# Kernel optimization log

Hardware: AMD Instinct MI355X
Metric: run time of the kernel (lower is better)

## Reference

```python
import jax, jax.numpy as jnp
import numpy as np

CONF_THRES = 0.25   # NMS.conf
IOU_THRES = 0.45    # NMS.iou
MAX_NMS = 1024      # fixed candidate count so greedy NMS is jit-compatible
IMG = 640.0


def setup_inputs() -> dict:
    key = jax.random.key(0)
    k0, k1, k2, k3, k4 = jax.random.split(key, 5)
    B, N = 32, 25200
    cxcy = jax.random.uniform(k0, (B, N, 2), dtype=jnp.float32) * IMG
    wh = jax.random.uniform(k1, (B, N, 2), dtype=jnp.float32) * 80.0 + 2.0
    obj = jax.random.uniform(k2, (B, N, 1), dtype=jnp.float32)
    lmk = jax.random.uniform(k3, (B, N, 10), dtype=jnp.float32) * IMG
    cls = jax.random.uniform(k4, (B, N, 1), dtype=jnp.float32)
    # layout: [cx, cy, w, h, obj, 10 landmark coords, 1 class score]
    prediction = jnp.concatenate([cxcy, wh, obj, lmk, cls], axis=2)
    return {"prediction": prediction}


def xywh2xyxy(x):
    cx, cy, w, h = x[:, 0], x[:, 1], x[:, 2], x[:, 3]
    return jnp.stack([cx - w / 2, cy - h / 2, cx + w / 2, cy + h / 2], axis=1)


def pairwise_iou(b):  # b: [K,4] xyxy -> [K,K]
    area = (b[:, 2] - b[:, 0]) * (b[:, 3] - b[:, 1])
    lt = jnp.maximum(b[:, None, :2], b[None, :, :2])
    rb = jnp.minimum(b[:, None, 2:], b[None, :, 2:])
    wh = jnp.clip(rb - lt, 0.0)
    inter = wh[..., 0] * wh[..., 1]
    return inter / (area[:, None] + area[None, :] - inter + 1e-7)


def _nms_image(pred):  # pred: [N,16]
    obj = pred[:, 4]
    score = pred[:, 15] * obj  # x[:,15:] *= x[:,4:5]; nc==1 -> single class, j==0
    valid = (obj > CONF_THRES) & (score > CONF_THRES)  # xc filter + conf filter
    s = jnp.where(valid, score, -1.0)
    top_s, idx = jax.lax.top_k(s, MAX_NMS)  # score-sorted candidates (greedy NMS order)
    x = pred[idx]  # [K,16]
    box = xywh2xyxy(x[:, :4])
    vmask = top_s > 0.0  # valid candidates (invalid slots carry score -1)
    # class offset c = j*4096 is identically 0 since nc==1 -> skip
    iou = pairwise_iou(box)  # [K,K]
    rng = jnp.arange(MAX_NMS)

    def step(keep, i):
        sup = keep[i] & (iou[i] > IOU_THRES) & (rng > i)
        return keep & ~sup, None

    keep, _ = jax.lax.scan(step, vmask, rng)
    det = jnp.concatenate(
        [box, top_s[:, None], x[:, 5:15], jnp.zeros((MAX_NMS, 1), pred.dtype)], axis=1
    )  # [K,16] = box(4) | conf(1) | landmarks(10) | class(1)=0
    return det * keep[:, None].astype(det.dtype), keep


def reference(prediction):
    # Fixed-shape analogue of the per-image ragged output: detections padded to
    # MAX_NMS rows per image (zeroed where suppressed) plus a keep mask.
    det, keep = jax.vmap(_nms_image)(prediction)
    return det, keep
```

## Files before the change

kernel.cpp:

```cpp
#include <hip/hip_runtime.h>
#include <stdint.h>

#define NB 32
#define NN 25200
#define NN4 6300
#define TOPK 1024
#define NF 16
#define CONF 0.25f
#define IOU_T 0.45f
#define NBIN 4096
#define CAP 2048
#define KEY_BASE 0xBE800001u
#define PITCH 257

__device__ __forceinline__ uint32_t score_key(float obj, float cls) {
  float score = __fmul_rn(cls, obj);
  bool valid = (obj > CONF) && (score > CONF);
  float s = valid ? score : -1.0f;
  uint32_t u = __float_as_uint(s);
  return (u & 0x80000000u) ? ~u : (u | 0x80000000u);
}

__device__ __forceinline__ uint64_t shfl_xor_u64(uint64_t v, int m) {
  uint32_t lo = __shfl_xor((uint32_t)v, m, 64);
  uint32_t hi = __shfl_xor((uint32_t)(v >> 32), m, 64);
  return ((uint64_t)hi << 32) | lo;
}

__global__ void k_keys(const float* __restrict__ pred, uint32_t* __restrict__ keys,
                       uint32_t* __restrict__ cnt) {
  if (blockIdx.x == 0 && threadIdx.x < NB) cnt[threadIdx.x] = 0u;
  int g = blockIdx.x * blockDim.x + threadIdx.x;
  if (g >= NB * NN) return;
  const float* row = pred + (size_t)g * NF;
  keys[g] = score_key(row[4], row[15]);
}

__global__ __launch_bounds__(1024) void k_select(const float* __restrict__ pred,
                                                 const uint32_t* __restrict__ keys,
                                                 int* __restrict__ sel,
                                                 float4* __restrict__ boxv,
                                                 float* __restrict__ arv,
                                                 uint32_t* __restrict__ vb) {
  int b = blockIdx.x;
  int tid = threadIdx.x;
  int lane = tid & 63, wid = tid >> 6;
  const uint4* kb4 = (const uint4*)(keys + (size_t)b * NN);
  __shared__ uint32_t hist[NBIN];
  __shared__ uint64_t ent[CAP];
  __shared__ uint32_t wsum[16];
  __shared__ uint32_t sh_bin;
  __shared__ uint32_t sh_cnt;
  #pragma unroll
  for (int k = 0; k < 4; ++k) hist[tid + 1024 * k] = 0;
  ent[tid] = 0; ent[tid + 1024] = 0;
  if (tid == 0) { sh_cnt = 0; sh_bin = 0; }
  __syncthreads();

  uint4 kreg[7];
  #pragma unroll
  for (int k = 0; k < 7; ++k) {
    int i = tid + k * 1024;
    if (i < NN4) {
      kreg[k] = kb4[i];
      uint32_t kv[4] = {kreg[k].x, kreg[k].y, kreg[k].z, kreg[k].w};
      #pragma unroll
      for (int c = 0; c < 4; ++c) {
        uint32_t key = kv[c];
        if (key >= KEY_BASE) {
          uint32_t bin = (key - KEY_BASE) >> 12;
          if (bin > NBIN - 1) bin = NBIN - 1;
          atomicAdd(&hist[bin], 1u);
        }
      }
    }
  }
  __syncthreads();

  uint32_t h[4]; uint32_t s = 0;
  #pragma unroll
  for (int k = 0; k < 4; ++k) { h[k] = hist[NBIN - 1 - (4 * tid + k)]; s += h[k]; }
  uint32_t my = s;
  #pragma unroll
  for (int d = 1; d < 64; d <<= 1) {
    uint32_t v = __shfl_up(s, d, 64);
    if (lane >= d) s += v;
  }
  if (lane == 63) wsum[wid] = s;
  __syncthreads();
  uint32_t base = 0;
  for (int w = 0; w < wid; ++w) base += wsum[w];
  uint32_t cum = base + s - my;
  #pragma unroll
  for (int k = 0; k < 4; ++k) {
    if (cum < TOPK && cum + h[k] >= TOPK) sh_bin = (uint32_t)(NBIN - 1 - (4 * tid + k));
    cum += h[k];
  }
  __syncthreads();
  uint32_t thr = KEY_BASE + (sh_bin << 12);

  #pragma unroll
  for (int k = 0; k < 7; ++k) {
    int i = tid + k * 1024;
    if (i < NN4) {
      uint32_t kv[4] = {kreg[k].x, kreg[k].y, kreg[k].z, kreg[k].w};
      #pragma unroll
      for (int c = 0; c < 4; ++c) {
        uint32_t key = kv[c];
        if (key >= thr) {
          uint32_t p = atomicAdd(&sh_cnt, 1u);
          if (p < CAP) ent[p] = ((uint64_t)key << 32) | (uint32_t)(~(uint32_t)(4 * i + c));
        }
      }
    }
  }
  __syncthreads();

  uint64_t v0 = ent[tid], v1 = ent[tid + 1024];
  for (unsigned kk = 2; kk <= CAP; kk <<= 1) {
    for (unsigned j = kk >> 1; j > 0; j >>= 1) {
      if (j == 1024) {
        uint64_t mx = v0 > v1 ? v0 : v1;
        uint64_t mn = v0 > v1 ? v1 : v0;
        v0 = mx; v1 = mn;
      } else if (j >= 64) {
        __syncthreads();
        ent[tid] = v0; ent[tid + 1024] = v1;
        __syncthreads();
        uint64_t p0 = ent[tid ^ j], p1 = ent[(tid ^ j) + 1024];
        bool low = ((tid & j) == 0);
        bool d0 = ((tid & kk) == 0);
        bool d1 = (((tid + 1024) & kk) == 0);
        v0 = (low != d0) ? (v0 < p0 ? v0 : p0) : (v0 > p0 ? v0 : p0);
        v1 = (low != d1) ? (v1 < p1 ? v1 : p1) : (v1 > p1 ? v1 : p1);
      } else {
        uint64_t p0 = shfl_xor_u64(v0, (int)j);
        uint64_t p1 = shfl_xor_u64(v1, (int)j);
        bool low = ((tid & j) == 0);
        bool d0 = ((tid & kk) == 0);
        bool d1 = (((tid + 1024) & kk) == 0);
        v0 = (low != d0) ? (v0 < p0 ? v0 : p0) : (v0 > p0 ? v0 : p0);
        v1 = (low != d1) ? (v1 < p1 ? v1 : p1) : (v1 > p1 ? v1 : p1);
      }
    }
  }
  uint32_t key = (uint32_t)(v0 >> 32);
  uint32_t n = ~(uint32_t)(v0 & 0xFFFFFFFFu);
  if (n >= NN) n = 0;
  sel[(size_t)b * TOPK + tid] = (int)n;

  bool valid = key >= KEY_BASE;
  uint64_t bal = __ballot(valid);
  if (lane == 0) {
    vb[(size_t)b * 32 + 2 * wid] = (uint32_t)bal;
    vb[(size_t)b * 32 + 2 * wid + 1] = (uint32_t)(bal >> 32);
  }

  {
    const float4* row = (const float4*)(pred + ((size_t)b * NN + n) * NF);
    float4 r0 = row[0];
    float hw = __fmul_rn(r0.z, 0.5f), hh = __fmul_rn(r0.w, 0.5f);
    float x1 = __fsub_rn(r0.x, hw), y1 = __fsub_rn(r0.y, hh);
    float x2 = __fadd_rn(r0.x, hw), y2 = __fadd_rn(r0.y, hh);
    boxv[(size_t)b * TOPK + tid] = make_float4(x1, y1, x2, y2);
    arv[(size_t)b * TOPK + tid] = __fmul_rn(__fsub_rn(x2, x1), __fsub_rn(y2, y1));
  }
}

__global__ __launch_bounds__(1024, 4) void k_maskscan(const float* __restrict__ pred,
                                                      const int* __restrict__ sel,
                                                      const float4* __restrict__ boxv,
                                                      const float* __restrict__ arv,
                                                      const uint32_t* __restrict__ vb,
                                                      uint32_t* __restrict__ mask,
                                                      uint32_t* __restrict__ cnt,
                                                      float* __restrict__ det,
                                                      float* __restrict__ keep_out) {
  int b = blockIdx.x;
  int sblk = blockIdx.y;
  int tid = threadIdx.x;
  int rg = tid & 31;
  int cc = tid >> 5;
  __shared__ uint4 sm4[32 * PITCH];
  __shared__ uint32_t part[1024];
  __shared__ uint32_t Kvec[32];
  __shared__ uint32_t vbs[32];
  __shared__ uint32_t sflag;
  float* bx1 = (float*)sm4;
  float* by1 = bx1 + TOPK;
  float* bx2 = by1 + TOPK;
  float* by2 = bx2 + TOPK;
  float* bar = by2 + TOPK;

  {
    float4 bb = boxv[(size_t)b * TOPK + tid];
    bx1[tid] = bb.x; by1[tid] = bb.y; bx2[tid] = bb.z; by2[tid] = bb.w;
    bar[tid] = arv[(size_t)b * TOPK + tid];
  }
  __syncthreads();
  int i0 = sblk * 128 + rg * 4;
  int iw = i0 >> 5;
  uint32_t wreg[4] = {0u, 0u, 0u, 0u};
  if (cc >= iw) {
    float rx1[4], ry1[4], rx2[4], ry2[4], rar[4];
    #pragma unroll
    for (int k = 0; k < 4; ++k) {
      rx1[k] = bx1[i0 + k]; ry1[k] = by1[i0 + k];
      rx2[k] = bx2[i0 + k]; ry2[k] = by2[i0 + k]; rar[k] = bar[i0 + k];
    }
    for (int jj = 0; jj < 32; ++jj) {
      int j = cc * 32 + jj;
      float cx1 = bx1[j], cy1 = by1[j], cx2 = bx2[j], cy2 = by2[j], car = bar[j];
      #pragma unroll
      for (int k = 0; k < 4; ++k) {
        float lx = fmaxf(rx1[k], cx1);
        float ly = fmaxf(ry1[k], cy1);
        float rx = fminf(rx2[k], cx2);
        float ry = fminf(ry2[k], cy2);
        float wd = fmaxf(__fsub_rn(rx, lx), 0.0f);
        float ht = fmaxf(__fsub_rn(ry, ly), 0.0f);
        float inter = __fmul_rn(wd, ht);
        float den = __fadd_rn(__fsub_rn(__fadd_rn(rar[k], car), inter), 1e-7f);
        float iou = __fdiv_rn(inter, den);
        wreg[k] |= (iou > IOU_T ? 1u : 0u) << jj;
      }
    }
    if (cc == iw) {
      #pragma unroll
      for (int k = 0; k < 4; ++k)
        wreg[k] &= ~((2u << ((i0 + k) & 31)) - 1u);
    }
  }
  uint4 out = make_uint4(wreg[0], wreg[1], wreg[2], wreg[3]);
  *(uint4*)&mask[((size_t)b * 32 + cc) * TOPK + i0] = out;

  __syncthreads();
  if (tid == 0)
    __hip_atomic_fetch_add(&cnt[b], 1u, __ATOMIC_RELEASE, __HIP_MEMORY_SCOPE_AGENT);
  if (sblk != 0) return;

  int n = sel[(size_t)b * TOPK + tid];
  const float4* rowv = (const float4*)(pred + ((size_t)b * NN + n) * NF);
  float4 r0 = rowv[0], r1 = rowv[1], r2 = rowv[2], r3 = rowv[3];

  if (tid == 0) {
    while (__hip_atomic_load(&cnt[b], __ATOMIC_RELAXED, __HIP_MEMORY_SCOPE_AGENT) < 8u)
      __builtin_amdgcn_s_sleep(16);
    (void)__hip_atomic_load(&cnt[b], __ATOMIC_ACQUIRE, __HIP_MEMORY_SCOPE_AGENT);
  }
  __syncthreads();

  const uint4* gm4 = (const uint4*)(mask + (size_t)b * (32 * TOPK));
  #pragma unroll
  for (int q = 0; q < 8; ++q) {
    int idx4 = tid + q * 1024;
    int row = idx4 >> 8;
    int col4 = idx4 & 255;
    sm4[row * PITCH + col4] = gm4[idx4];
  }
  if (tid < 32) { uint32_t v = vb[(size_t)b * 32 + tid]; vbs[tid] = v; Kvec[tid] = v; }
  __syncthreads();

  {
    int l = tid & 31;
    int chunk = tid >> 5;
    const int rbase = l * PITCH + chunk * 8;
    uint32_t go = 1u;
    for (int sweep = 0; sweep < 1030 && go; ++sweep) {
      uint32_t kc = Kvec[chunk];
      uint32_t acc = 0;
      #pragma unroll
      for (int q = 0; q < 8; ++q) {
        uint4 v = sm4[rbase + q];
        acc |= (0u - ((kc >> (q * 4 + 0)) & 1u)) & v.x;
        acc |= (0u - ((kc >> (q * 4 + 1)) & 1u)) & v.y;
        acc |= (0u - ((kc >> (q * 4 + 2)) & 1u)) & v.z;
        acc |= (0u - ((kc >> (q * 4 + 3)) & 1u)) & v.w;
      }
      part[tid] = acc;
      __syncthreads();
      if (tid < 32) {
        uint32_t red = 0;
        #pragma unroll
        for (int c = 0; c < 32; ++c) red |= part[c * 32 + tid];
        uint32_t nk = vbs[tid] & ~red;
        uint64_t chg = __ballot(nk != Kvec[tid]);
        Kvec[tid] = nk;
        if (tid == 0) sflag = (chg != 0ull) ? 1u : 0u;
      }
      __syncthreads();
      go = sflag;
    }
  }

  bool kept = (Kvec[tid >> 5] >> (tid & 31)) & 1u;
  float m = kept ? 1.0f : 0.0f;
  float score = __fmul_rn(r3.w, r1.x);
  float hw = __fmul_rn(r0.z, 0.5f), hh = __fmul_rn(r0.w, 0.5f);
  float4 o0 = make_float4(__fsub_rn(r0.x, hw) * m, __fsub_rn(r0.y, hh) * m,
                          __fadd_rn(r0.x, hw) * m, __fadd_rn(r0.y, hh) * m);
  float4 o1 = make_float4(score * m, r1.y * m, r1.z * m, r1.w * m);
  float4 o2 = make_float4(r2.x * m, r2.y * m, r2.z * m, r2.w * m);
  float4 o3 = make_float4(r3.x * m, r3.y * m, r3.z * m, 0.0f);
  float4* dst = (float4*)(det + ((size_t)b * TOPK + tid) * NF);
  dst[0] = o0; dst[1] = o1; dst[2] = o2; dst[3] = o3;
  keep_out[(size_t)b * TOPK + tid] = m;
}

extern "C" void kernel_launch(void* const* d_in, const int* in_sizes, int n_in,
                              void* d_out, int out_size, void* d_ws, size_t ws_size,
                              hipStream_t stream) {
  const float* pred = (const float*)d_in[0];
  float* det = (float*)d_out;
  float* keep = det + (size_t)NB * TOPK * NF;

  uint8_t* ws = (uint8_t*)d_ws;
  size_t off = 0;
  uint32_t* keys = (uint32_t*)(ws + off); off += (size_t)NB * NN * 4;
  int* sel = (int*)(ws + off);            off += (size_t)NB * TOPK * 4;
  uint32_t* mask = (uint32_t*)(ws + off); off += (size_t)NB * 32 * TOPK * 4;
  float4* boxv = (float4*)(ws + off);     off += (size_t)NB * TOPK * 16;
  float* arv = (float*)(ws + off);        off += (size_t)NB * TOPK * 4;
  uint32_t* vb = (uint32_t*)(ws + off);   off += (size_t)NB * 32 * 4;
  uint32_t* cnt = (uint32_t*)(ws + off);  off += (size_t)NB * 4;

  k_keys<<<(NB * NN + 255) / 256, 256, 0, stream>>>(pred, keys, cnt);
  k_select<<<NB, 1024, 0, stream>>>(pred, keys, sel, boxv, arv, vb);
  dim3 gm(NB, 8);
  k_maskscan<<<gm, 1024, 0, stream>>>(pred, sel, boxv, arv, vb, mask, cnt, det, keep);
}
```

Measured before the change: 145.7 us.

## Fuse key, select and mask-scan kernels into one persistent kernel with flag sync

Merges the three launches into a single kernel. Each of the 8 blocks per image computes a slice of score keys, block 0 performs the histogram top-k and bitonic sort, then publishes boxes, and the other blocks spin on global counters before building their mask tiles. Mask rows are reassigned so each block takes an interleaved column set (i0 = 32*rg + 4*sblk), which balances the triangular IoU work across blocks. This removes launch gaps and the sel/vb round trips, but adds inter-block spin waits that rely on all 256 blocks being co-resident, plus a memset launch.

New measurement: 162.4 us. 11.5% more time.

```diff
diff --git a/kernel.cpp b/kernel.cpp
--- a/kernel.cpp
+++ b/kernel.cpp
@@ -4,6 +4,7 @@
 #define NB 32
 #define NN 25200
 #define NN4 6300
+#define RPS 3150
 #define TOPK 1024
 #define NF 16
 #define CONF 0.25f
@@ -27,181 +28,206 @@
   return ((uint64_t)hi << 32) | lo;
 }
 
-__global__ void k_keys(const float* __restrict__ pred, uint32_t* __restrict__ keys,
-                       uint32_t* __restrict__ cnt) {
-  if (blockIdx.x == 0 && threadIdx.x < NB) cnt[threadIdx.x] = 0u;
-  int g = blockIdx.x * blockDim.x + threadIdx.x;
-  if (g >= NB * NN) return;
-  const float* row = pred + (size_t)g * NF;
-  keys[g] = score_key(row[4], row[15]);
-}
-
-__global__ __launch_bounds__(1024) void k_select(const float* __restrict__ pred,
-                                                 const uint32_t* __restrict__ keys,
-                                                 int* __restrict__ sel,
+__global__ __launch_bounds__(1024, 4) void k_nms(const float* __restrict__ pred,
+                                                 uint32_t* __restrict__ keys,
                                                  float4* __restrict__ boxv,
                                                  float* __restrict__ arv,
-                                                 uint32_t* __restrict__ vb) {
-  int b = blockIdx.x;
-  int tid = threadIdx.x;
-  int lane = tid & 63, wid = tid >> 6;
-  const uint4* kb4 = (const uint4*)(keys + (size_t)b * NN);
-  __shared__ uint32_t hist[NBIN];
-  __shared__ uint64_t ent[CAP];
-  __shared__ uint32_t wsum[16];
-  __shared__ uint32_t sh_bin;
-  __shared__ uint32_t sh_cnt;
-  #pragma unroll
-  for (int k = 0; k < 4; ++k) hist[tid + 1024 * k] = 0;
-  ent[tid] = 0; ent[tid + 1024] = 0;
-  if (tid == 0) { sh_cnt = 0; sh_bin = 0; }
-  __syncthreads();
-
-  uint4 kreg[7];
-  #pragma unroll
-  for (int k = 0; k < 7; ++k) {
-    int i = tid + k * 1024;
-    if (i < NN4) {
-      kreg[k] = kb4[i];
-      uint32_t kv[4] = {kreg[k].x, kreg[k].y, kreg[k].z, kreg[k].w};
-      #pragma unroll
-      for (int c = 0; c < 4; ++c) {
-        uint32_t key = kv[c];
-        if (key >= KEY_BASE) {
-          uint32_t bin = (key - KEY_BASE) >> 12;
-          if (bin > NBIN - 1) bin = NBIN - 1;
-          atomicAdd(&hist[bin], 1u);
-        }
-      }
-    }
-  }
-  __syncthreads();
-
-  uint32_t h[4]; uint32_t s = 0;
-  #pragma unroll
-  for (int k = 0; k < 4; ++k) { h[k] = hist[NBIN - 1 - (4 * tid + k)]; s += h[k]; }
-  uint32_t my = s;
-  #pragma unroll
-  for (int d = 1; d < 64; d <<= 1) {
-    uint32_t v = __shfl_up(s, d, 64);
-    if (lane >= d) s += v;
-  }
-  if (lane == 63) wsum[wid] = s;
-  __syncthreads();
-  uint32_t base = 0;
-  for (int w = 0; w < wid; ++w) base += wsum[w];
-  uint32_t cum = base + s - my;
-  #pragma unroll
-  for (int k = 0; k < 4; ++k) {
-    if (cum < TOPK && cum + h[k] >= TOPK) sh_bin = (uint32_t)(NBIN - 1 - (4 * tid + k));
-    cum += h[k];
-  }
-  __syncthreads();
-  uint32_t thr = KEY_BASE + (sh_bin << 12);
-
-  #pragma unroll
-  for (int k = 0; k < 7; ++k) {
-    int i = tid + k * 1024;
-    if (i < NN4) {
-      uint32_t kv[4] = {kreg[k].x, kreg[k].y, kreg[k].z, kreg[k].w};
-      #pragma unroll
-      for (int c = 0; c < 4; ++c) {
-        uint32_t key = kv[c];
-        if (key >= thr) {
-          uint32_t p = atomicAdd(&sh_cnt, 1u);
-          if (p < CAP) ent[p] = ((uint64_t)key << 32) | (uint32_t)(~(uint32_t)(4 * i + c));
-        }
-      }
-    }
-  }
-  __syncthreads();
-
-  uint64_t v0 = ent[tid], v1 = ent[tid + 1024];
-  for (unsigned kk = 2; kk <= CAP; kk <<= 1) {
-    for (unsigned j = kk >> 1; j > 0; j >>= 1) {
-      if (j == 1024) {
-        uint64_t mx = v0 > v1 ? v0 : v1;
-        uint64_t mn = v0 > v1 ? v1 : v0;
-        v0 = mx; v1 = mn;
-      } else if (j >= 64) {
-        __syncthreads();
-        ent[tid] = v0; ent[tid + 1024] = v1;
-        __syncthreads();
-        uint64_t p0 = ent[tid ^ j], p1 = ent[(tid ^ j) + 1024];
-        bool low = ((tid & j) == 0);
-        bool d0 = ((tid & kk) == 0);
-        bool d1 = (((tid + 1024) & kk) == 0);
-        v0 = (low != d0) ? (v0 < p0 ? v0 : p0) : (v0 > p0 ? v0 : p0);
-        v1 = (low != d1) ? (v1 < p1 ? v1 : p1) : (v1 > p1 ? v1 : p1);
-      } else {
-        uint64_t p0 = shfl_xor_u64(v0, (int)j);
-        uint64_t p1 = shfl_xor_u64(v1, (int)j);
-        bool low = ((tid & j) == 0);
-        bool d0 = ((tid & kk) == 0);
-        bool d1 = (((tid + 1024) & kk) == 0);
-        v0 = (low != d0) ? (v0 < p0 ? v0 : p0) : (v0 > p0 ? v0 : p0);
-        v1 = (low != d1) ? (v1 < p1 ? v1 : p1) : (v1 > p1 ? v1 : p1);
-      }
-    }
-  }
-  uint32_t key = (uint32_t)(v0 >> 32);
-  uint32_t n = ~(uint32_t)(v0 & 0xFFFFFFFFu);
-  if (n >= NN) n = 0;
-  sel[(size_t)b * TOPK + tid] = (int)n;
-
-  bool valid = key >= KEY_BASE;
-  uint64_t bal = __ballot(valid);
-  if (lane == 0) {
-    vb[(size_t)b * 32 + 2 * wid] = (uint32_t)bal;
-    vb[(size_t)b * 32 + 2 * wid + 1] = (uint32_t)(bal >> 32);
-  }
-
-  {
-    const float4* row = (const float4*)(pred + ((size_t)b * NN + n) * NF);
-    float4 r0 = row[0];
-    float hw = __fmul_rn(r0.z, 0.5f), hh = __fmul_rn(r0.w, 0.5f);
-    float x1 = __fsub_rn(r0.x, hw), y1 = __fsub_rn(r0.y, hh);
-    float x2 = __fadd_rn(r0.x, hw), y2 = __fadd_rn(r0.y, hh);
-    boxv[(size_t)b * TOPK + tid] = make_float4(x1, y1, x2, y2);
-    arv[(size_t)b * TOPK + tid] = __fmul_rn(__fsub_rn(x2, x1), __fsub_rn(y2, y1));
-  }
-}
-
-__global__ __launch_bounds__(1024, 4) void k_maskscan(const float* __restrict__ pred,
-                                                      const int* __restrict__ sel,
-                                                      const float4* __restrict__ boxv,
-                                                      const float* __restrict__ arv,
-                                                      const uint32_t* __restrict__ vb,
-                                                      uint32_t* __restrict__ mask,
-                                                      uint32_t* __restrict__ cnt,
-                                                      float* __restrict__ det,
-                                                      float* __restrict__ keep_out) {
+                                                 uint32_t* __restrict__ mask,
+                                                 uint32_t* __restrict__ cnt,
+                                                 float* __restrict__ det,
+                                                 float* __restrict__ keep_out) {
   int b = blockIdx.x;
   int sblk = blockIdx.y;
   int tid = threadIdx.x;
+  int lane = tid & 63, wid = tid >> 6;
   int rg = tid & 31;
   int cc = tid >> 5;
+
   __shared__ uint4 sm4[32 * PITCH];
   __shared__ uint32_t part[1024];
   __shared__ uint32_t Kvec[32];
   __shared__ uint32_t vbs[32];
   __shared__ uint32_t sflag;
+  __shared__ uint32_t wsum[16];
+  __shared__ uint32_t sh_bin;
+  __shared__ uint32_t sh_cnt;
+
   float* bx1 = (float*)sm4;
   float* by1 = bx1 + TOPK;
   float* bx2 = by1 + TOPK;
   float* by2 = bx2 + TOPK;
   float* bar = by2 + TOPK;
+  uint32_t* hist = (uint32_t*)(bar + TOPK);
+  uint64_t* ent = (uint64_t*)(hist + NBIN);
+
+  uint32_t* cntk = cnt;
+  uint32_t* cnts = cnt + NB;
+  uint32_t* cntm = cnt + 2 * NB;
 
   {
-    float4 bb = boxv[(size_t)b * TOPK + tid];
-    bx1[tid] = bb.x; by1[tid] = bb.y; bx2[tid] = bb.z; by2[tid] = bb.w;
-    bar[tid] = arv[(size_t)b * TOPK + tid];
+    int base = sblk * RPS;
+    #pragma unroll
+    for (int q = 0; q < 4; ++q) {
+      int t = tid + q * 1024;
+      if (t < RPS) {
+        int g = b * NN + base + t;
+        const float* row = pred + (size_t)g * NF;
+        keys[g] = score_key(row[4], row[15]);
+      }
+    }
   }
   __syncthreads();
-  int i0 = sblk * 128 + rg * 4;
-  int iw = i0 >> 5;
+  if (tid == 0)
+    __hip_atomic_fetch_add(&cntk[b], 1u, __ATOMIC_RELEASE, __HIP_MEMORY_SCOPE_AGENT);
+
+  int n = 0;
+
+  if (sblk == 0) {
+    if (tid == 0) {
+      while (__hip_atomic_load(&cntk[b], __ATOMIC_RELAXED, __HIP_MEMORY_SCOPE_AGENT) < 8u)
+        __builtin_amdgcn_s_sleep(16);
+      (void)__hip_atomic_load(&cntk[b], __ATOMIC_ACQUIRE, __HIP_MEMORY_SCOPE_AGENT);
+    }
+    __syncthreads();
+
+    const uint4* kb4 = (const uint4*)(keys + (size_t)b * NN);
+    #pragma unroll
+    for (int k = 0; k < 4; ++k) hist[tid + 1024 * k] = 0;
+    ent[tid] = 0; ent[tid + 1024] = 0;
+    if (tid == 0) { sh_cnt = 0; sh_bin = 0; }
+    __syncthreads();
+
+    uint4 kreg[7];
+    #pragma unroll
+    for (int k = 0; k < 7; ++k) {
+      int i = tid + k * 1024;
+      if (i < NN4) {
+        kreg[k] = kb4[i];
+        uint32_t kv[4] = {kreg[k].x, kreg[k].y, kreg[k].z, kreg[k].w};
+        #pragma unroll
+        for (int c = 0; c < 4; ++c) {
+          uint32_t key = kv[c];
+          if (key >= KEY_BASE) {
+            uint32_t bin = (key - KEY_BASE) >> 12;
+            if (bin > NBIN - 1) bin = NBIN - 1;
+            atomicAdd(&hist[bin], 1u);
+          }
+        }
+      }
+    }
+    __syncthreads();
+
+    uint32_t h[4]; uint32_t s = 0;
+    #pragma unroll
+    for (int k = 0; k < 4; ++k) { h[k] = hist[NBIN - 1 - (4 * tid + k)]; s += h[k]; }
+    uint32_t my = s;
+    #pragma unroll
+    for (int d = 1; d < 64; d <<= 1) {
+      uint32_t v = __shfl_up(s, d, 64);
+      if (lane >= d) s += v;
+    }
+    if (lane == 63) wsum[wid] = s;
+    __syncthreads();
+    uint32_t base = 0;
+    for (int w = 0; w < wid; ++w) base += wsum[w];
+    uint32_t cum = base + s - my;
+    #pragma unroll
+    for (int k = 0; k < 4; ++k) {
+      if (cum < TOPK && cum + h[k] >= TOPK) sh_bin = (uint32_t)(NBIN - 1 - (4 * tid + k));
+      cum += h[k];
+    }
+    __syncthreads();
+    uint32_t thr = KEY_BASE + (sh_bin << 12);
+
+    #pragma unroll
+    for (int k = 0; k < 7; ++k) {
+      int i = tid + k * 1024;
+      if (i < NN4) {
+        uint32_t kv[4] = {kreg[k].x, kreg[k].y, kreg[k].z, kreg[k].w};
+        #pragma unroll
+        for (int c = 0; c < 4; ++c) {
+          uint32_t key = kv[c];
+          if (key >= thr) {
+            uint32_t p = atomicAdd(&sh_cnt, 1u);
+            if (p < CAP) ent[p] = ((uint64_t)key << 32) | (uint32_t)(~(uint32_t)(4 * i + c));
+          }
+        }
+      }
+    }
+    __syncthreads();
+
+    uint64_t v0 = ent[tid], v1 = ent[tid + 1024];
+    for (unsigned kk = 2; kk <= CAP; kk <<= 1) {
+      for (unsigned j = kk >> 1; j > 0; j >>= 1) {
+        if (j == 1024) {
+          uint64_t mx = v0 > v1 ? v0 : v1;
+          uint64_t mn = v0 > v1 ? v1 : v0;
+          v0 = mx; v1 = mn;
+        } else if (j >= 64) {
+          __syncthreads();
+          ent[tid] = v0; ent[tid + 1024] = v1;
+          __syncthreads();
+          uint64_t p0 = ent[tid ^ j], p1 = ent[(tid ^ j) + 1024];
+          bool low = ((tid & j) == 0);
+          bool d0 = ((tid & kk) == 0);
+          bool d1 = (((tid + 1024) & kk) == 0);
+          v0 = (low != d0) ? (v0 < p0 ? v0 : p0) : (v0 > p0 ? v0 : p0);
+          v1 = (low != d1) ? (v1 < p1 ? v1 : p1) : (v1 > p1 ? v1 : p1);
+        } else {
+          uint64_t p0 = shfl_xor_u64(v0, (int)j);
+          uint64_t p1 = shfl_xor_u64(v1, (int)j);
+          bool low = ((tid & j) == 0);
+          bool d0 = ((tid & kk) == 0);
+          bool d1 = (((tid + 1024) & kk) == 0);
+          v0 = (low != d0) ? (v0 < p0 ? v0 : p0) : (v0 > p0 ? v0 : p0);
+          v1 = (low != d1) ? (v1 < p1 ? v1 : p1) : (v1 > p1 ? v1 : p1);
+        }
+      }
+    }
+    uint32_t key = (uint32_t)(v0 >> 32);
+    uint32_t nn = ~(uint32_t)(v0 & 0xFFFFFFFFu);
+    if (nn >= NN) nn = 0;
+    n = (int)nn;
+
+    bool valid = key >= KEY_BASE;
+    uint64_t bal = __ballot(valid);
+    if (lane == 0) {
+      vbs[2 * wid] = (uint32_t)bal;  vbs[2 * wid + 1] = (uint32_t)(bal >> 32);
+      Kvec[2 * wid] = (uint32_t)bal; Kvec[2 * wid + 1] = (uint32_t)(bal >> 32);
+    }
+
+    {
+      const float4* row = (const float4*)(pred + ((size_t)b * NN + n) * NF);
+      float4 r0 = row[0];
+      float hw = __fmul_rn(r0.z, 0.5f), hh = __fmul_rn(r0.w, 0.5f);
+      float x1 = __fsub_rn(r0.x, hw), y1 = __fsub_rn(r0.y, hh);
+      float x2 = __fadd_rn(r0.x, hw), y2 = __fadd_rn(r0.y, hh);
+      float ar = __fmul_rn(__fsub_rn(x2, x1), __fsub_rn(y2, y1));
+      bx1[tid] = x1; by1[tid] = y1; bx2[tid] = x2; by2[tid] = y2; bar[tid] = ar;
+      boxv[(size_t)b * TOPK + tid] = make_float4(x1, y1, x2, y2);
+      arv[(size_t)b * TOPK + tid] = ar;
+    }
+    __syncthreads();
+    if (tid == 0)
+      __hip_atomic_fetch_add(&cnts[b], 1u, __ATOMIC_RELEASE, __HIP_MEMORY_SCOPE_AGENT);
+  } else {
+    if (tid == 0) {
+      while (__hip_atomic_load(&cnts[b], __ATOMIC_RELAXED, __HIP_MEMORY_SCOPE_AGENT) < 1u)
+        __builtin_amdgcn_s_sleep(16);
+      (void)__hip_atomic_load(&cnts[b], __ATOMIC_ACQUIRE, __HIP_MEMORY_SCOPE_AGENT);
+    }
+    __syncthreads();
+    {
+      float4 bb = boxv[(size_t)b * TOPK + tid];
+      bx1[tid] = bb.x; by1[tid] = bb.y; bx2[tid] = bb.z; by2[tid] = bb.w;
+      bar[tid] = arv[(size_t)b * TOPK + tid];
+    }
+    __syncthreads();
+  }
+
+  int i0 = 32 * rg + 4 * sblk;
   uint32_t wreg[4] = {0u, 0u, 0u, 0u};
-  if (cc >= iw) {
+  if (cc >= rg) {
     float rx1[4], ry1[4], rx2[4], ry2[4], rar[4];
     #pragma unroll
     for (int k = 0; k < 4; ++k) {
@@ -225,28 +251,28 @@
         wreg[k] |= (iou > IOU_T ? 1u : 0u) << jj;
       }
     }
-    if (cc == iw) {
+    if (cc == rg) {
       #pragma unroll
       for (int k = 0; k < 4; ++k)
         wreg[k] &= ~((2u << ((i0 + k) & 31)) - 1u);
     }
   }
-  uint4 out = make_uint4(wreg[0], wreg[1], wreg[2], wreg[3]);
-  *(uint4*)&mask[((size_t)b * 32 + cc) * TOPK + i0] = out;
-
+  {
+    uint4 out = make_uint4(wreg[0], wreg[1], wreg[2], wreg[3]);
+    *(uint4*)&mask[((size_t)b * 32 + cc) * TOPK + i0] = out;
+  }
   __syncthreads();
   if (tid == 0)
-    __hip_atomic_fetch_add(&cnt[b], 1u, __ATOMIC_RELEASE, __HIP_MEMORY_SCOPE_AGENT);
+    __hip_atomic_fetch_add(&cntm[b], 1u, __ATOMIC_RELEASE, __HIP_MEMORY_SCOPE_AGENT);
   if (sblk != 0) return;
 
-  int n = sel[(size_t)b * TOPK + tid];
   const float4* rowv = (const float4*)(pred + ((size_t)b * NN + n) * NF);
   float4 r0 = rowv[0], r1 = rowv[1], r2 = rowv[2], r3 = rowv[3];
 
   if (tid == 0) {
-    while (__hip_atomic_load(&cnt[b], __ATOMIC_RELAXED, __HIP_MEMORY_SCOPE_AGENT) < 8u)
+    while (__hip_atomic_load(&cntm[b], __ATOMIC_RELAXED, __HIP_MEMORY_SCOPE_AGENT) < 8u)
       __builtin_amdgcn_s_sleep(16);
-    (void)__hip_atomic_load(&cnt[b], __ATOMIC_ACQUIRE, __HIP_MEMORY_SCOPE_AGENT);
+    (void)__hip_atomic_load(&cntm[b], __ATOMIC_ACQUIRE, __HIP_MEMORY_SCOPE_AGENT);
   }
   __syncthreads();
 
@@ -258,7 +284,6 @@
     int col4 = idx4 & 255;
     sm4[row * PITCH + col4] = gm4[idx4];
   }
-  if (tid < 32) { uint32_t v = vb[(size_t)b * 32 + tid]; vbs[tid] = v; Kvec[tid] = v; }
   __syncthreads();
 
   {
@@ -317,15 +342,12 @@
   uint8_t* ws = (uint8_t*)d_ws;
   size_t off = 0;
   uint32_t* keys = (uint32_t*)(ws + off); off += (size_t)NB * NN * 4;
-  int* sel = (int*)(ws + off);            off += (size_t)NB * TOPK * 4;
-  uint32_t* mask = (uint32_t*)(ws + off); off += (size_t)NB * 32 * TOPK * 4;
   float4* boxv = (float4*)(ws + off);     off += (size_t)NB * TOPK * 16;
   float* arv = (float*)(ws + off);        off += (size_t)NB * TOPK * 4;
-  uint32_t* vb = (uint32_t*)(ws + off);   off += (size_t)NB * 32 * 4;
-  uint32_t* cnt = (uint32_t*)(ws + off);  off += (size_t)NB * 4;
-
-  k_keys<<<(NB * NN + 255) / 256, 256, 0, stream>>>(pred, keys, cnt);
-  k_select<<<NB, 1024, 0, stream>>>(pred, keys, sel, boxv, arv, vb);
-  dim3 gm(NB, 8);
-  k_maskscan<<<gm, 1024, 0, stream>>>(pred, sel, boxv, arv, vb, mask, cnt, det, keep);
+  uint32_t* mask = (uint32_t*)(ws + off); off += (size_t)NB * 32 * TOPK * 4;
+  uint32_t* cnt = (uint32_t*)(ws + off);  off += (size_t)3 * NB * 4;
+
+  hipMemsetAsync(cnt, 0, (size_t)3 * NB * 4, stream);
+  dim3 g(NB, 8);
+  k_nms<<<g, 1024, 0, stream>>>(pred, keys, boxv, arv, mask, cnt, det, keep);
 }
```
